# Optimization experiments

Hardware: AMD Instinct MI355X
Metric: run time of the kernel (lower is better)

## Reference

```python
import jax, jax.numpy as jnp
import numpy as np

B, N, V = 8, 2000, 2000
K = 100            # local_size
EMB = 128          # ff_hidden_dim
PENALTY = -1e9
EPS = 1e-5         # InstanceNorm eps


def setup_inputs() -> dict:
    key = jax.random.key(0)
    ks = jax.random.split(key, 16)
    s = 0.02
    return {
        "dist": jax.random.uniform(ks[0], (B, N, V), dtype=jnp.float32),
        "theta": jax.random.normal(ks[1], (B, N, V), dtype=jnp.float32),
        "scale": jax.random.uniform(ks[2], (B, N, 1), dtype=jnp.float32),
        # Linear params stored [in, out]
        "w1": jax.random.normal(ks[3], (2 * K + 1, EMB), dtype=jnp.float32) * s,
        "b1": jnp.zeros((EMB,), jnp.float32),
        "w2": jax.random.normal(ks[4], (EMB, 2 * EMB), dtype=jnp.float32) * s,
        "b2": jnp.zeros((2 * EMB,), jnp.float32),
        "w3": jax.random.normal(ks[5], (2 * EMB, EMB), dtype=jnp.float32) * s,
        "b3": jnp.zeros((EMB,), jnp.float32),
        "w4": jax.random.normal(ks[6], (EMB, K), dtype=jnp.float32) * s,
        "b4": jnp.zeros((K,), jnp.float32),
        "gamma": jnp.ones((2 * EMB,), jnp.float32),   # InstanceNorm affine weight
        "beta": jnp.zeros((2 * EMB,), jnp.float32),   # InstanceNorm affine bias
    }


def reference(dist, theta, scale, w1, b1, w2, b2, w3, b3, w4, b4, gamma, beta):
    # --- topk smallest distances (ascending) + gather theta ---
    neg_vals, idx = jax.lax.top_k(-dist, K)          # [B,N,K]
    sorted_dist = -neg_vals                           # ascending k smallest
    sorted_dist = sorted_dist / jnp.max(sorted_dist, axis=-1, keepdims=True)
    sorted_theta = jnp.take_along_axis(theta, idx, axis=-1)  # [B,N,K]

    # --- small MLP with InstanceNorm over the node dim ---
    x_in = jnp.concatenate([sorted_dist, sorted_theta, scale], axis=-1)  # [B,N,2K+1]
    emb = jax.nn.relu(x_in @ w1 + b1)                 # [B,N,EMB]
    h = jax.nn.relu(emb @ w2 + b2)                    # [B,N,2*EMB]
    # InstanceNorm1d: normalize each channel over the length (node) dim, biased var
    mean = jnp.mean(h, axis=1, keepdims=True)
    var = jnp.var(h, axis=1, keepdims=True)
    h = (h - mean) * jax.lax.rsqrt(var + EPS) * gamma + beta
    emb = jax.nn.relu(h @ w3 + b3)                    # [B,N,EMB]
    out = (emb @ w4 + b4) - sorted_dist               # [B,N,K]

    # --- scatter into penalty-initialized matrix ---
    out_mat = jnp.full((B, N, V), PENALTY, dtype=dist.dtype)
    b_ix = jnp.arange(B)[:, None, None]
    n_ix = jnp.arange(N)[None, :, None]
    return out_mat.at[b_ix, n_ix, idx].set(out)
```

## Files before the change

kernel.cpp:

```cpp
#include <hip/hip_runtime.h>
#include <hip/hip_bf16.h>

#define BB 8
#define NN 2000
#define VV 2000
#define KK 100
#define EMB 128
#define PENALTY -1e9f
#define NBIN 512
#define BINSCALE 2048.0f
#define CAP 200
#define XPAD 224

typedef __attribute__((ext_vector_type(8))) short short8;
typedef __attribute__((ext_vector_type(4))) float f32x4;

#define WB() __builtin_amdgcn_wave_barrier()

__device__ __forceinline__ unsigned short bf16rne(float f) {
    unsigned u = __float_as_uint(f);
    u += 0x7FFF + ((u >> 16) & 1);
    return (unsigned short)(u >> 16);
}
__device__ __forceinline__ float bf2f(unsigned short s) {
    return __uint_as_float((unsigned)s << 16);
}

#define FORALL_VALS(BODY)                                                    \
    _Pragma("unroll") for (int c = 0; c < 8; ++c) {                          \
        { const float fv = v4[c].x; const int e = (c * 64 + lane) * 4 + 0; BODY } \
        { const float fv = v4[c].y; const int e = (c * 64 + lane) * 4 + 1; BODY } \
        { const float fv = v4[c].z; const int e = (c * 64 + lane) * 4 + 2; BODY } \
        { const float fv = v4[c].w; const int e = (c * 64 + lane) * 4 + 3; BODY } \
    }

__global__ __launch_bounds__(256) void wpack_kernel(
    const float* __restrict__ w1, const float* __restrict__ w2,
    const float* __restrict__ w3, const float* __restrict__ w4,
    unsigned short* __restrict__ pw1, unsigned short* __restrict__ pw2,
    unsigned short* __restrict__ pw3, unsigned short* __restrict__ pw4)
{
    const int bt = blockIdx.x;
    const int t = threadIdx.x;
    for (int e = t; e < 512; e += 256) {
        int lane = e >> 3, j = e & 7;
        int kk = ((lane >> 4) << 3) + j;
        int nn = lane & 15;
        if (bt < 56) {
            int kt = bt >> 3, nt = bt & 7;
            int k = kt * 32 + kk, n = nt * 16 + nn;
            float f = (k < 201) ? w1[k * 128 + n] : 0.f;
            pw1[bt * 512 + e] = bf16rne(f);
        } else if (bt < 120) {
            int bb = bt - 56, kt = bb >> 4, nt = bb & 15;
            pw2[bb * 512 + e] = bf16rne(w2[(kt * 32 + kk) * 256 + nt * 16 + nn]);
        } else if (bt < 184) {
            int bb = bt - 120, kt = bb >> 3, nt = bb & 7;
            pw3[bb * 512 + e] = bf16rne(w3[(kt * 32 + kk) * 128 + nt * 16 + nn]);
        } else {
            int bb = bt - 184, kt = bb / 7, nt = bb % 7;
            int n = nt * 16 + nn;
            float f = (n < 100) ? w4[(kt * 32 + kk) * 100 + n] : 0.f;
            pw4[bb * 512 + e] = bf16rne(f);
        }
    }
}

__global__ __launch_bounds__(256) void topk_kernel(
    const float* __restrict__ dist, const float* __restrict__ scale,
    unsigned short* __restrict__ xin, float* __restrict__ sdist,
    int* __restrict__ idxb)
{
    __shared__ __align__(16) unsigned hist[4][NBIN / 2];
    __shared__ __align__(16) unsigned snap[4][NBIN / 2];
    __shared__ unsigned long long comp[4][CAP];
    __shared__ unsigned long long comp2[4][KK];
    __shared__ int sh_cnt[4], sh_ntie[4], sh_kth[4];
    __shared__ unsigned sh_pref[4];
    __shared__ int sh_tie[4][64];

    const int t = threadIdx.x;
    const int w = t >> 6, lane = t & 63;
    const int row = blockIdx.x * 4 + w;
    const float4* d4 = (const float4*)(dist + (size_t)row * VV);

    float4 v4[8];
#pragma unroll
    for (int c = 0; c < 7; ++c) v4[c] = d4[c * 64 + lane];
    v4[7] = (lane < 52) ? d4[448 + lane] : make_float4(2.f, 2.f, 2.f, 2.f);

#pragma unroll
    for (int i = 0; i < 4; ++i) hist[w][lane * 4 + i] = 0u;
    if (lane == 0) { sh_cnt[w] = 0; sh_ntie[w] = 0; }
    WB();

    FORALL_VALS({
        int b = (int)(fv * BINSCALE);
        b = b < 0 ? 0 : b;
        if (b < NBIN - 1)
            atomicAdd(&hist[w][b >> 1], 1u << ((b & 1) << 4));
        (void)e;
    });
    WB();

    unsigned cw0 = hist[w][lane * 4 + 0];
    unsigned cw1 = hist[w][lane * 4 + 1];
    unsigned cw2 = hist[w][lane * 4 + 2];
    unsigned cw3 = hist[w][lane * 4 + 3];
    unsigned tot = (cw0 & 0xFFFFu) + (cw0 >> 16) + (cw1 & 0xFFFFu) + (cw1 >> 16) +
                   (cw2 & 0xFFFFu) + (cw2 >> 16) + (cw3 & 0xFFFFu) + (cw3 >> 16);
    unsigned incl = tot;
#pragma unroll
    for (int off = 1; off < 64; off <<= 1) {
        unsigned v = __shfl_up(incl, (unsigned)off);
        if (lane >= off) incl += v;
    }
    unsigned run = incl - tot;

    int myBt = -1, myM = 0;
#pragma unroll
    for (int i = 0; i < 4; ++i) {
        unsigned cwi = (i == 0) ? cw0 : (i == 1) ? cw1 : (i == 2) ? cw2 : cw3;
        unsigned c0 = cwi & 0xFFFFu, c1 = cwi >> 16;
        unsigned st0 = run, st1 = run + c0;
        if (myBt < 0 && st0 < KK && st0 + c0 >= KK) {
            myBt = lane * 8 + 2 * i; myM = (int)(st0 + c0);
        }
        if (myBt < 0 && st1 < KK && st1 + c1 >= KK) {
            myBt = lane * 8 + 2 * i + 1; myM = (int)(st1 + c1);
        }
        unsigned packed = st0 | (st1 << 16);
        hist[w][lane * 4 + i] = packed;
        snap[w][lane * 4 + i] = packed;
        run = st1 + c1;
    }
    WB();

    unsigned long long bl = __ballot(myBt >= 0);
    int Bt, m;
    if (bl != 0ull) {
        int src = __ffsll(bl) - 1;
        Bt = __shfl(myBt, src);
        m = __shfl(myM, src);
    } else {
        Bt = NBIN - 1;
        m = 100000;
    }

    if (m <= CAP) {
        FORALL_VALS({
            int b = (int)(fv * BINSCALE);
            b = b < 0 ? 0 : (b > NBIN - 1 ? NBIN - 1 : b);
            if (b <= Bt) {
                int sh = (b & 1) << 4;
                unsigned old = atomicAdd(&hist[w][b >> 1], 1u << sh);
                int slot = (int)((old >> sh) & 0xFFFFu);
                comp[w][slot] =
                    ((unsigned long long)__float_as_uint(fv) << 32) | (unsigned)e;
            }
        });
        WB();
        for (int o = lane; o < m; o += 64) {
            unsigned long long key = comp[w][o];
            float fv = __uint_as_float((unsigned)(key >> 32));
            int b = (int)(fv * BINSCALE);
            b = b < 0 ? 0 : (b > NBIN - 1 ? NBIN - 1 : b);
            int sh = (b & 1) << 4;
            unsigned e0 = (hist[w][b >> 1] >> sh) & 0xFFFFu;
            unsigned s0 = (snap[w][b >> 1] >> sh) & 0xFFFFu;
            int r = (int)s0;
            for (unsigned s = s0; s < e0; ++s) r += (comp[w][s] < key);
            if (r < KK) comp2[w][r] = key;
        }
    } else {
        FORALL_VALS({
            int b = (int)(fv * BINSCALE);
            b = b < 0 ? 0 : (b > NBIN - 1 ? NBIN - 1 : b);
            if (b < Bt) {
                int pos = atomicAdd(&sh_cnt[w], 1);
                if (pos < CAP)
                    comp[w][pos] =
                        ((unsigned long long)__float_as_uint(fv) << 32) | (unsigned)e;
            }
        });
        WB();
        int nless = sh_cnt[w];
        if (lane == 0) { sh_pref[w] = 0u; sh_kth[w] = KK - nless; }
        WB();
        for (int p = 0; p < 4; ++p) {
#pragma unroll
            for (int i = 0; i < 4; ++i) hist[w][lane * 4 + i] = 0u;
            WB();
            const int shift = 24 - 8 * p;
            const unsigned pref = sh_pref[w];
            FORALL_VALS({
                int b = (int)(fv * BINSCALE);
                b = b < 0 ? 0 : (b > NBIN - 1 ? NBIN - 1 : b);
                if (b == Bt) {
                    unsigned k = __float_as_uint(fv);
                    bool ok = (p == 0) || ((k >> (shift + 8)) == pref);
                    if (ok) atomicAdd(&hist[w][(k >> shift) & 255u], 1u);
                }
                (void)e;
            });
            WB();
            if (lane == 0) {
                int kth = sh_kth[w];
                unsigned cum = 0;
                int b = 0;
                for (; b < 256; ++b) {
                    unsigned cc = hist[w][b];
                    if (cum + cc >= (unsigned)kth) break;
                    cum += cc;
                }
                sh_pref[w] = (pref << 8) | (unsigned)b;
                sh_kth[w] = kth - (int)cum;
            }
            WB();
        }
        const unsigned T = sh_pref[w];
        const int need2 = sh_kth[w];
        FORALL_VALS({
            int b = (int)(fv * BINSCALE);
            b = b < 0 ? 0 : (b > NBIN - 1 ? NBIN - 1 : b);
            if (b == Bt) {
                unsigned k = __float_as_uint(fv);
                if (k < T) {
                    int pos = atomicAdd(&sh_cnt[w], 1);
                    if (pos < CAP)
                        comp[w][pos] = ((unsigned long long)k << 32) | (unsigned)e;
                } else if (k == T) {
                    int q = atomicAdd(&sh_ntie[w], 1);
                    if (q < 64) sh_tie[w][q] = e;
                }
            }
        });
        WB();
        if (lane == 0) {
            int nl2 = sh_cnt[w];
            int nt = sh_ntie[w] < 64 ? sh_ntie[w] : 64;
            for (int i = 1; i < nt; ++i) {
                int v = sh_tie[w][i], j2 = i - 1;
                while (j2 >= 0 && sh_tie[w][j2] > v) {
                    sh_tie[w][j2 + 1] = sh_tie[w][j2];
                    --j2;
                }
                sh_tie[w][j2 + 1] = v;
            }
            for (int i = 0; i < need2; ++i)
                comp[w][nl2 + i] =
                    ((unsigned long long)T << 32) | (unsigned)sh_tie[w][i];
            sh_cnt[w] = nl2 + need2;
        }
        WB();
        const int mm = sh_cnt[w];
        for (int o = lane; o < mm; o += 64) {
            unsigned long long key = comp[w][o];
            int r = 0;
            for (int j2 = 0; j2 < mm; ++j2) {
                unsigned long long cj = comp[w][j2];
                r += (cj < key) || (cj == key && j2 < o);
            }
            if (r < KK) comp2[w][r] = key;
        }
    }
    WB();

    const float Tf = __uint_as_float((unsigned)(comp2[w][KK - 1] >> 32));
    const float invT = 1.0f / Tf;
    for (int o = lane; o < KK; o += 64) {
        unsigned long long c = comp2[w][o];
        unsigned kbits = (unsigned)(c >> 32);
        int id = (int)(c & 0xFFFFFFFFu);
        float nv = __uint_as_float(kbits) * invT;
        xin[(size_t)row * XPAD + o] = bf16rne(nv);
        sdist[(size_t)row * KK + o] = nv;
        idxb[(size_t)row * KK + o] = id;
    }
    if (lane == 0) xin[(size_t)row * XPAD + 200] = bf16rne(scale[row]);
    else if (lane < 24) xin[(size_t)row * XPAD + 200 + lane] = 0;
}

__global__ __launch_bounds__(256) void gather_kernel(
    const float* __restrict__ theta, const int* __restrict__ idxb,
    unsigned short* __restrict__ xin)
{
    const int i = blockIdx.x * 256 + threadIdx.x;
    const int row = i / KK;
    const int k = i - row * KK;
    const int id = idxb[i];
    float v = theta[(size_t)row * VV + id];
    xin[(size_t)row * XPAD + 100 + k] = bf16rne(v);
}

__global__ __launch_bounds__(256) void fused12_mfma(
    const unsigned short* __restrict__ xin, const unsigned short* __restrict__ pw1,
    const float* __restrict__ b1, const unsigned short* __restrict__ pw2,
    const float* __restrict__ b2, unsigned short* __restrict__ h)
{
    __shared__ unsigned short c1s[64][136];
    const int t = threadIdx.x;
    const int w = t >> 6, l = t & 63;
    const int m0 = blockIdx.x * 64;
    const int lr = l & 15, lg = l >> 4;

    f32x4 acc[8] = {};
    const short8* arow = (const short8*)(xin + (size_t)(m0 + 16 * w + lr) * XPAD);
    const short8* pw1v = (const short8*)pw1;
#pragma unroll
    for (int kt = 0; kt < 7; ++kt) {
        short8 a = arow[kt * 4 + lg];
#pragma unroll
        for (int nt = 0; nt < 8; ++nt) {
            short8 b = pw1v[(kt * 8 + nt) * 64 + l];
            acc[nt] = __builtin_amdgcn_mfma_f32_16x16x32_bf16(a, b, acc[nt], 0, 0, 0);
        }
    }
#pragma unroll
    for (int nt = 0; nt < 8; ++nt) {
        int col = nt * 16 + lr;
        float bb = b1[col];
#pragma unroll
        for (int r = 0; r < 4; ++r) {
            float v = fmaxf(acc[nt][r] + bb, 0.f);
            c1s[16 * w + lg * 4 + r][col] = bf16rne(v);
        }
    }
    __syncthreads();

    f32x4 acc2[16] = {};
    const short8* pw2v = (const short8*)pw2;
#pragma unroll
    for (int kt = 0; kt < 4; ++kt) {
        short8 a = *(const short8*)&c1s[16 * w + lr][kt * 32 + lg * 8];
#pragma unroll
        for (int nt = 0; nt < 16; ++nt) {
            short8 b = pw2v[(kt * 16 + nt) * 64 + l];
            acc2[nt] = __builtin_amdgcn_mfma_f32_16x16x32_bf16(a, b, acc2[nt], 0, 0, 0);
        }
    }
#pragma unroll
    for (int nt = 0; nt < 16; ++nt) {
        int col = nt * 16 + lr;
        float bb = b2[col];
#pragma unroll
        for (int r = 0; r < 4; ++r) {
            float v = fmaxf(acc2[nt][r] + bb, 0.f);
            h[(size_t)(m0 + 16 * w + lg * 4 + r) * 256 + col] = bf16rne(v);
        }
    }
}

#define NCHUNK 25
#define CHUNK (NN / NCHUNK)

__global__ __launch_bounds__(256) void stats_partial(
    const unsigned short* __restrict__ h, float* __restrict__ part)
{
    const int b = blockIdx.x, ch = blockIdx.y, c = threadIdx.x;
    const unsigned short* base = h + ((size_t)b * NN + (size_t)ch * CHUNK) * 256 + c;
    float s = 0.f, s2 = 0.f;
    for (int n = 0; n < CHUNK; ++n) {
        float v = bf2f(base[(size_t)n * 256]);
        s += v;
        s2 += v * v;
    }
    size_t o = (((size_t)b * NCHUNK + ch) * 256 + c) * 2;
    part[o] = s;
    part[o + 1] = s2;
}

__global__ __launch_bounds__(256) void stats_final(
    const float* __restrict__ part, const float* __restrict__ gamma,
    const float* __restrict__ beta, float* __restrict__ scv,
    float* __restrict__ shv)
{
    const int b = blockIdx.x, c = threadIdx.x;
    float s = 0.f, s2 = 0.f;
    for (int ch = 0; ch < NCHUNK; ++ch) {
        size_t o = (((size_t)b * NCHUNK + ch) * 256 + c) * 2;
        s += part[o];
        s2 += part[o + 1];
    }
    const float inv = 1.0f / (float)NN;
    float mean = s * inv;
    float var = s2 * inv - mean * mean;
    float rs = rsqrtf(var + 1e-5f);
    float sc = gamma[c] * rs;
    scv[b * 256 + c] = sc;
    shv[b * 256 + c] = beta[c] - mean * sc;
}

__global__ __launch_bounds__(256) void fused34_mfma(
    const unsigned short* __restrict__ h, const unsigned short* __restrict__ pw3,
    const float* __restrict__ b3, const unsigned short* __restrict__ pw4,
    const float* __restrict__ b4, const float* __restrict__ scv,
    const float* __restrict__ shv, const float* __restrict__ sdist,
    const int* __restrict__ idxb, float* __restrict__ out)
{
    __shared__ __align__(16) char uni[64 * 100 * 4];
    __shared__ __align__(16) unsigned bm[64][64];
    __shared__ __align__(16) unsigned short wpref[64][64];
    unsigned short (*c1s)[136] = (unsigned short (*)[136])uni;
    float (*valbuf)[100] = (float (*)[100])uni;

    const int t = threadIdx.x;
    const int w = t >> 6, l = t & 63;
    const int m0 = blockIdx.x * 64;
    const int lr = l & 15, lg = l >> 4;

    for (int i = t; i < 64 * 64; i += 256) ((unsigned*)bm)[i] = 0u;
    __syncthreads();

    for (int i = t; i < 64 * KK; i += 256) {
        int rrow = i / KK;
        int id = idxb[(size_t)(m0 + rrow) * KK + (i - rrow * KK)];
        atomicOr(&bm[rrow][id >> 5], 1u << (id & 31));
    }

    const int myrow = m0 + 16 * w + lr;
    const int mybatch = myrow / NN;

    f32x4 acc[8] = {};
    const short8* hrow = (const short8*)(h + (size_t)myrow * 256);
    const short8* pw3v = (const short8*)pw3;
#pragma unroll
    for (int kt = 0; kt < 8; ++kt) {
        int k0 = kt * 32 + lg * 8;
        short8 hv = hrow[kt * 4 + lg];
        const float4* scp = (const float4*)(scv + mybatch * 256 + k0);
        const float4* shp = (const float4*)(shv + mybatch * 256 + k0);
        float4 sc0 = scp[0], sc1 = scp[1];
        float4 sh0 = shp[0], sh1 = shp[1];
        short8 a;
        a[0] = (short)bf16rne(fmaf(bf2f((unsigned short)hv[0]), sc0.x, sh0.x));
        a[1] = (short)bf16rne(fmaf(bf2f((unsigned short)hv[1]), sc0.y, sh0.y));
        a[2] = (short)bf16rne(fmaf(bf2f((unsigned short)hv[2]), sc0.z, sh0.z));
        a[3] = (short)bf16rne(fmaf(bf2f((unsigned short)hv[3]), sc0.w, sh0.w));
        a[4] = (short)bf16rne(fmaf(bf2f((unsigned short)hv[4]), sc1.x, sh1.x));
        a[5] = (short)bf16rne(fmaf(bf2f((unsigned short)hv[5]), sc1.y, sh1.y));
        a[6] = (short)bf16rne(fmaf(bf2f((unsigned short)hv[6]), sc1.z, sh1.z));
        a[7] = (short)bf16rne(fmaf(bf2f((unsigned short)hv[7]), sc1.w, sh1.w));
#pragma unroll
        for (int nt = 0; nt < 8; ++nt) {
            short8 b = pw3v[(kt * 8 + nt) * 64 + l];
            acc[nt] = __builtin_amdgcn_mfma_f32_16x16x32_bf16(a, b, acc[nt], 0, 0, 0);
        }
    }
    __syncthreads();

    if (t < 64) {
        unsigned run = 0;
#pragma unroll
        for (int wd = 0; wd < 63; ++wd) {
            wpref[t][wd] = (unsigned short)run;
            run += (unsigned)__popc(bm[t][wd]);
        }
        wpref[t][63] = (unsigned short)run;
    }

#pragma unroll
    for (int nt = 0; nt < 8; ++nt) {
        int col = nt * 16 + lr;
        float bb = b3[col];
#pragma unroll
        for (int r = 0; r < 4; ++r) {
            float v = fmaxf(acc[nt][r] + bb, 0.f);
            c1s[16 * w + lg * 4 + r][col] = bf16rne(v);
        }
    }
    __syncthreads();

    f32x4 acc2[7] = {};
    const short8* pw4v = (const short8*)pw4;
#pragma unroll
    for (int kt = 0; kt < 4; ++kt) {
        short8 a = *(const short8*)&c1s[16 * w + lr][kt * 32 + lg * 8];
#pragma unroll
        for (int nt = 0; nt < 7; ++nt) {
            short8 b = pw4v[(kt * 7 + nt) * 64 + l];
            acc2[nt] = __builtin_amdgcn_mfma_f32_16x16x32_bf16(a, b, acc2[nt], 0, 0, 0);
        }
    }
    __syncthreads();

#pragma unroll
    for (int nt = 0; nt < 7; ++nt) {
        int col = nt * 16 + lr;
        if (col < KK) {
            float bb = b4[col];
#pragma unroll
            for (int r = 0; r < 4; ++r) {
                int r4 = 16 * w + lg * 4 + r;
                int mrow = m0 + r4;
                float v = acc2[nt][r] + bb - sdist[(size_t)mrow * KK + col];
                int id = idxb[(size_t)mrow * KK + col];
                int wd = id >> 5;
                int irank = (int)wpref[r4][wd] +
                            __popc(bm[r4][wd] & ((1u << (id & 31)) - 1u));
                valbuf[r4][irank] = v;
            }
        }
    }
    __syncthreads();

    for (int i = t; i < 64 * (VV / 4); i += 256) {
        int rrow = i / (VV / 4);
        int p = i - rrow * (VV / 4);
        int v0 = p * 4;
        unsigned word = bm[rrow][v0 >> 5];
        int sh = v0 & 31;
        int racc = (int)wpref[rrow][v0 >> 5] + __popc(word & ((1u << sh) - 1u));
        float4 o;
        unsigned b0 = (word >> sh) & 1u;
        o.x = b0 ? valbuf[rrow][racc] : PENALTY; racc += b0;
        unsigned b1_ = (word >> (sh + 1)) & 1u;
        o.y = b1_ ? valbuf[rrow][racc] : PENALTY; racc += b1_;
        unsigned b2_ = (word >> (sh + 2)) & 1u;
        o.z = b2_ ? valbuf[rrow][racc] : PENALTY; racc += b2_;
        unsigned b3_ = (word >> (sh + 3)) & 1u;
        o.w = b3_ ? valbuf[rrow][racc] : PENALTY;
        ((float4*)(out + (size_t)(m0 + rrow) * VV))[p] = o;
    }
}

extern "C" void kernel_launch(void* const* d_in, const int* in_sizes, int n_in,
                              void* d_out, int out_size, void* d_ws, size_t ws_size,
                              hipStream_t stream)
{
    const float* dist  = (const float*)d_in[0];
    const float* theta = (const float*)d_in[1];
    const float* scale = (const float*)d_in[2];
    const float* w1 = (const float*)d_in[3];
    const float* b1 = (const float*)d_in[4];
    const float* w2 = (const float*)d_in[5];
    const float* b2 = (const float*)d_in[6];
    const float* w3 = (const float*)d_in[7];
    const float* b3 = (const float*)d_in[8];
    const float* w4 = (const float*)d_in[9];
    const float* b4 = (const float*)d_in[10];
    const float* gamma = (const float*)d_in[11];
    const float* beta  = (const float*)d_in[12];
    float* out = (float*)d_out;

    const int M = BB * NN;

    char* p = (char*)d_ws;
    unsigned short* xin = (unsigned short*)p;       p += (size_t)M * XPAD * 2;
    unsigned short* h   = (unsigned short*)p;       p += (size_t)M * 256 * 2;
    float* sdist = (float*)p;                       p += (size_t)M * KK * 4;
    int*   idxb  = (int*)p;                         p += (size_t)M * KK * 4;
    float* part  = (float*)p;                       p += (size_t)BB * NCHUNK * 256 * 2 * 4;
    float* scv   = (float*)p;                       p += 8 * 256 * 4;
    float* shv   = (float*)p;                       p += 8 * 256 * 4;
    unsigned short* pw1 = (unsigned short*)p;       p += 56 * 512 * 2;
    unsigned short* pw2 = (unsigned short*)p;       p += 64 * 512 * 2;
    unsigned short* pw3 = (unsigned short*)p;       p += 64 * 512 * 2;
    unsigned short* pw4 = (unsigned short*)p;       p += 28 * 512 * 2;

    wpack_kernel<<<212, 256, 0, stream>>>(w1, w2, w3, w4, pw1, pw2, pw3, pw4);

    topk_kernel<<<M / 4, 256, 0, stream>>>(dist, scale, xin, sdist, idxb);

    gather_kernel<<<(M * KK) / 256, 256, 0, stream>>>(theta, idxb, xin);

    fused12_mfma<<<M / 64, 256, 0, stream>>>(xin, pw1, b1, pw2, b2, h);

    stats_partial<<<dim3(BB, NCHUNK), 256, 0, stream>>>(h, part);
    stats_final<<<BB, 256, 0, stream>>>(part, gamma, beta, scv, shv);

    fused34_mfma<<<M / 64, 256, 0, stream>>>(h, pw3, b3, pw4, b4, scv, shv,
                                             sdist, idxb, out);
}
```

Before: 138.3 us.

## Fold weight packing into topk launch, add fast small-bin path, shrink sdist/idx to 16-bit

Merges the weight-packing kernel into the top-k kernel as extra leading blocks, which removes one launch. Adds a per-row fast path: when at least K values fall below a small threshold, bins are cached as packed bytes so the second histogram pass does not recompute them. Stores sorted distances as bf16 and indices as uint16, halving intermediate traffic for the gather and final kernels. The bf16 sdist subtraction changes precision slightly and adds a divergent branch in top-k.

```diff
diff --git a/kernel.cpp b/kernel.cpp
--- a/kernel.cpp
+++ b/kernel.cpp
@@ -11,6 +11,9 @@
 #define BINSCALE 2048.0f
 #define CAP 200
 #define XPAD 224
+#define SMALLTHR (255.0f / 2048.0f)
+#define NWPACK 212
+#define TOPKB (BB * NN / 4)
 
 typedef __attribute__((ext_vector_type(8))) short short8;
 typedef __attribute__((ext_vector_type(4))) float f32x4;
@@ -27,49 +30,21 @@
 }
 
 #define FORALL_VALS(BODY)                                                    \
-    _Pragma("unroll") for (int c = 0; c < 8; ++c) {                          \
-        { const float fv = v4[c].x; const int e = (c * 64 + lane) * 4 + 0; BODY } \
-        { const float fv = v4[c].y; const int e = (c * 64 + lane) * 4 + 1; BODY } \
-        { const float fv = v4[c].z; const int e = (c * 64 + lane) * 4 + 2; BODY } \
-        { const float fv = v4[c].w; const int e = (c * 64 + lane) * 4 + 3; BODY } \
-    }
-
-__global__ __launch_bounds__(256) void wpack_kernel(
+    _Pragma("unroll") for (int ci = 0; ci < 8; ++ci) {                       \
+        { const int j = 0; const float fv = v4[ci].x; const int e = (ci * 64 + lane) * 4 + 0; BODY } \
+        { const int j = 1; const float fv = v4[ci].y; const int e = (ci * 64 + lane) * 4 + 1; BODY } \
+        { const int j = 2; const float fv = v4[ci].z; const int e = (ci * 64 + lane) * 4 + 2; BODY } \
+        { const int j = 3; const float fv = v4[ci].w; const int e = (ci * 64 + lane) * 4 + 3; BODY } \
+    }
+
+__global__ __launch_bounds__(256) void topk_kernel(
+    const float* __restrict__ dist, const float* __restrict__ scale,
+    unsigned short* __restrict__ xin, unsigned short* __restrict__ sdist,
+    unsigned short* __restrict__ idxb,
     const float* __restrict__ w1, const float* __restrict__ w2,
     const float* __restrict__ w3, const float* __restrict__ w4,
     unsigned short* __restrict__ pw1, unsigned short* __restrict__ pw2,
     unsigned short* __restrict__ pw3, unsigned short* __restrict__ pw4)
-{
-    const int bt = blockIdx.x;
-    const int t = threadIdx.x;
-    for (int e = t; e < 512; e += 256) {
-        int lane = e >> 3, j = e & 7;
-        int kk = ((lane >> 4) << 3) + j;
-        int nn = lane & 15;
-        if (bt < 56) {
-            int kt = bt >> 3, nt = bt & 7;
-            int k = kt * 32 + kk, n = nt * 16 + nn;
-            float f = (k < 201) ? w1[k * 128 + n] : 0.f;
-            pw1[bt * 512 + e] = bf16rne(f);
-        } else if (bt < 120) {
-            int bb = bt - 56, kt = bb >> 4, nt = bb & 15;
-            pw2[bb * 512 + e] = bf16rne(w2[(kt * 32 + kk) * 256 + nt * 16 + nn]);
-        } else if (bt < 184) {
-            int bb = bt - 120, kt = bb >> 3, nt = bb & 7;
-            pw3[bb * 512 + e] = bf16rne(w3[(kt * 32 + kk) * 128 + nt * 16 + nn]);
-        } else {
-            int bb = bt - 184, kt = bb / 7, nt = bb % 7;
-            int n = nt * 16 + nn;
-            float f = (n < 100) ? w4[(kt * 32 + kk) * 100 + n] : 0.f;
-            pw4[bb * 512 + e] = bf16rne(f);
-        }
-    }
-}
-
-__global__ __launch_bounds__(256) void topk_kernel(
-    const float* __restrict__ dist, const float* __restrict__ scale,
-    unsigned short* __restrict__ xin, float* __restrict__ sdist,
-    int* __restrict__ idxb)
 {
     __shared__ __align__(16) unsigned hist[4][NBIN / 2];
     __shared__ __align__(16) unsigned snap[4][NBIN / 2];
@@ -80,25 +55,63 @@
     __shared__ int sh_tie[4][64];
 
     const int t = threadIdx.x;
+
+    if (blockIdx.x < NWPACK) {
+        const int bt = blockIdx.x;
+        for (int e = t; e < 512; e += 256) {
+            int lane = e >> 3, j = e & 7;
+            int kk = ((lane >> 4) << 3) + j;
+            int nn = lane & 15;
+            if (bt < 56) {
+                int kt = bt >> 3, nt = bt & 7;
+                int k = kt * 32 + kk, n = nt * 16 + nn;
+                float f = (k < 201) ? w1[k * 128 + n] : 0.f;
+                pw1[bt * 512 + e] = bf16rne(f);
+            } else if (bt < 120) {
+                int bb = bt - 56, kt = bb >> 4, nt = bb & 15;
+                pw2[bb * 512 + e] = bf16rne(w2[(kt * 32 + kk) * 256 + nt * 16 + nn]);
+            } else if (bt < 184) {
+                int bb = bt - 120, kt = bb >> 3, nt = bb & 7;
+                pw3[bb * 512 + e] = bf16rne(w3[(kt * 32 + kk) * 128 + nt * 16 + nn]);
+            } else {
+                int bb = bt - 184, kt = bb / 7, nt = bb % 7;
+                int n = nt * 16 + nn;
+                float f = (n < 100) ? w4[(kt * 32 + kk) * 100 + n] : 0.f;
+                pw4[bb * 512 + e] = bf16rne(f);
+            }
+        }
+        return;
+    }
+
     const int w = t >> 6, lane = t & 63;
-    const int row = blockIdx.x * 4 + w;
+    const int row = (blockIdx.x - NWPACK) * 4 + w;
     const float4* d4 = (const float4*)(dist + (size_t)row * VV);
 
     float4 v4[8];
 #pragma unroll
     for (int c = 0; c < 7; ++c) v4[c] = d4[c * 64 + lane];
     v4[7] = (lane < 52) ? d4[448 + lane] : make_float4(2.f, 2.f, 2.f, 2.f);
+
+    int nsmall = 0;
+    FORALL_VALS({ nsmall += (fv < SMALLTHR) ? 1 : 0; (void)e; (void)j; (void)ci; });
+#pragma unroll
+    for (int off = 1; off < 64; off <<= 1) nsmall += __shfl_xor(nsmall, off);
+    const bool fast = (nsmall >= KK);
 
 #pragma unroll
     for (int i = 0; i < 4; ++i) hist[w][lane * 4 + i] = 0u;
     if (lane == 0) { sh_cnt[w] = 0; sh_ntie[w] = 0; }
     WB();
 
+    unsigned bcache[8];
     FORALL_VALS({
         int b = (int)(fv * BINSCALE);
-        b = b < 0 ? 0 : b;
-        if (b < NBIN - 1)
-            atomicAdd(&hist[w][b >> 1], 1u << ((b & 1) << 4));
+        b = b < 0 ? 0 : (b > NBIN - 1 ? NBIN - 1 : b);
+        int bb = b > 255 ? 255 : b;
+        if (j == 0) bcache[ci] = (unsigned)bb;
+        else bcache[ci] |= (unsigned)bb << (8 * j);
+        bool doh = fast ? (b < 255) : (b < NBIN - 1);
+        if (doh) atomicAdd(&hist[w][b >> 1], 1u << ((b & 1) << 4));
         (void)e;
     });
     WB();
@@ -149,8 +162,12 @@
 
     if (m <= CAP) {
         FORALL_VALS({
-            int b = (int)(fv * BINSCALE);
-            b = b < 0 ? 0 : (b > NBIN - 1 ? NBIN - 1 : b);
+            int b;
+            if (fast) b = (int)((bcache[ci] >> (8 * j)) & 255u);
+            else {
+                b = (int)(fv * BINSCALE);
+                b = b < 0 ? 0 : (b > NBIN - 1 ? NBIN - 1 : b);
+            }
             if (b <= Bt) {
                 int sh = (b & 1) << 4;
                 unsigned old = atomicAdd(&hist[w][b >> 1], 1u << sh);
@@ -182,6 +199,7 @@
                     comp[w][pos] =
                         ((unsigned long long)__float_as_uint(fv) << 32) | (unsigned)e;
             }
+            (void)j; (void)ci;
         });
         WB();
         int nless = sh_cnt[w];
@@ -201,7 +219,7 @@
                     bool ok = (p == 0) || ((k >> (shift + 8)) == pref);
                     if (ok) atomicAdd(&hist[w][(k >> shift) & 255u], 1u);
                 }
-                (void)e;
+                (void)e; (void)j; (void)ci;
             });
             WB();
             if (lane == 0) {
@@ -234,6 +252,7 @@
                     if (q < 64) sh_tie[w][q] = e;
                 }
             }
+            (void)j; (void)ci;
         });
         WB();
         if (lane == 0) {
@@ -272,23 +291,23 @@
         unsigned long long c = comp2[w][o];
         unsigned kbits = (unsigned)(c >> 32);
         int id = (int)(c & 0xFFFFFFFFu);
-        float nv = __uint_as_float(kbits) * invT;
-        xin[(size_t)row * XPAD + o] = bf16rne(nv);
-        sdist[(size_t)row * KK + o] = nv;
-        idxb[(size_t)row * KK + o] = id;
+        unsigned short nb = bf16rne(__uint_as_float(kbits) * invT);
+        xin[(size_t)row * XPAD + o] = nb;
+        sdist[(size_t)row * KK + o] = nb;
+        idxb[(size_t)row * KK + o] = (unsigned short)id;
     }
     if (lane == 0) xin[(size_t)row * XPAD + 200] = bf16rne(scale[row]);
     else if (lane < 24) xin[(size_t)row * XPAD + 200 + lane] = 0;
 }
 
 __global__ __launch_bounds__(256) void gather_kernel(
-    const float* __restrict__ theta, const int* __restrict__ idxb,
+    const float* __restrict__ theta, const unsigned short* __restrict__ idxb,
     unsigned short* __restrict__ xin)
 {
     const int i = blockIdx.x * 256 + threadIdx.x;
     const int row = i / KK;
     const int k = i - row * KK;
-    const int id = idxb[i];
+    const int id = (int)idxb[i];
     float v = theta[(size_t)row * VV + id];
     xin[(size_t)row * XPAD + 100 + k] = bf16rne(v);
 }
@@ -395,8 +414,8 @@
     const unsigned short* __restrict__ h, const unsigned short* __restrict__ pw3,
     const float* __restrict__ b3, const unsigned short* __restrict__ pw4,
     const float* __restrict__ b4, const float* __restrict__ scv,
-    const float* __restrict__ shv, const float* __restrict__ sdist,
-    const int* __restrict__ idxb, float* __restrict__ out)
+    const float* __restrict__ shv, const unsigned short* __restrict__ sdist,
+    const unsigned short* __restrict__ idxb, float* __restrict__ out)
 {
     __shared__ __align__(16) char uni[64 * 100 * 4];
     __shared__ __align__(16) unsigned bm[64][64];
@@ -414,7 +433,7 @@
 
     for (int i = t; i < 64 * KK; i += 256) {
         int rrow = i / KK;
-        int id = idxb[(size_t)(m0 + rrow) * KK + (i - rrow * KK)];
+        int id = (int)idxb[(size_t)(m0 + rrow) * KK + (i - rrow * KK)];
         atomicOr(&bm[rrow][id >> 5], 1u << (id & 31));
     }
 
@@ -493,8 +512,9 @@
             for (int r = 0; r < 4; ++r) {
                 int r4 = 16 * w + lg * 4 + r;
                 int mrow = m0 + r4;
-                float v = acc2[nt][r] + bb - sdist[(size_t)mrow * KK + col];
-                int id = idxb[(size_t)mrow * KK + col];
+                float v = acc2[nt][r] + bb -
+                          bf2f(sdist[(size_t)mrow * KK + col]);
+                int id = (int)idxb[(size_t)mrow * KK + col];
                 int wd = id >> 5;
                 int irank = (int)wpref[r4][wd] +
                             __popc(bm[r4][wd] & ((1u << (id & 31)) - 1u));
@@ -546,10 +566,10 @@
     const int M = BB * NN;
 
     char* p = (char*)d_ws;
-    unsigned short* xin = (unsigned short*)p;       p += (size_t)M * XPAD * 2;
-    unsigned short* h   = (unsigned short*)p;       p += (size_t)M * 256 * 2;
-    float* sdist = (float*)p;                       p += (size_t)M * KK * 4;
-    int*   idxb  = (int*)p;                         p += (size_t)M * KK * 4;
+    unsigned short* xin   = (unsigned short*)p;     p += (size_t)M * XPAD * 2;
+    unsigned short* h     = (unsigned short*)p;     p += (size_t)M * 256 * 2;
+    unsigned short* sdist = (unsigned short*)p;     p += (size_t)M * KK * 2;
+    unsigned short* idxb  = (unsigned short*)p;     p += (size_t)M * KK * 2;
     float* part  = (float*)p;                       p += (size_t)BB * NCHUNK * 256 * 2 * 4;
     float* scv   = (float*)p;                       p += 8 * 256 * 4;
     float* shv   = (float*)p;                       p += 8 * 256 * 4;
@@ -558,9 +578,9 @@
     unsigned short* pw3 = (unsigned short*)p;       p += 64 * 512 * 2;
     unsigned short* pw4 = (unsigned short*)p;       p += 28 * 512 * 2;
 
-    wpack_kernel<<<212, 256, 0, stream>>>(w1, w2, w3, w4, pw1, pw2, pw3, pw4);
-
-    topk_kernel<<<M / 4, 256, 0, stream>>>(dist, scale, xin, sdist, idxb);
+    topk_kernel<<<NWPACK + TOPKB, 256, 0, stream>>>(
+        dist, scale, xin, sdist, idxb,
+        w1, w2, w3, w4, pw1, pw2, pw3, pw4);
 
     gather_kernel<<<(M * KK) / 256, 256, 0, stream>>>(theta, idxb, xin);
 
```

After: 133.8 us. 3.3% less time.
